# Performance work log

Measured on AMD Instinct MI355X. Metric: run time of the kernel, lower is better.

Reference implementation:

```python
import jax, jax.numpy as jnp
import numpy as np

VOCAB, HIDDEN, NUM_LABELS = 400000, 300, 7
B, S = 256, 512


def setup_inputs() -> dict:
    key = jax.random.key(0)
    ks = jax.random.split(key, 8)
    return {
        "input_ids": jax.random.randint(ks[0], (B, S), 0, VOCAB, dtype=jnp.int64 if jax.config.jax_enable_x64 else jnp.int32).astype(jnp.int32),
        "attention_masks": jax.random.randint(ks[1], (B, S), 0, 2).astype(jnp.int32),
        "labels": jax.random.randint(ks[2], (B,), 0, NUM_LABELS).astype(jnp.int32),
        "drop_mask": jax.random.randint(ks[3], (B, S), 0, 2).astype(jnp.int32),
        "emb_table": jax.random.normal(ks[4], (VOCAB, HIDDEN), dtype=jnp.float32) * 0.1,
        "W1": jax.random.normal(ks[5], (HIDDEN, HIDDEN), dtype=jnp.float32) * 0.05,
        "b1": jnp.zeros((HIDDEN,), jnp.float32),
        "W2": jax.random.normal(ks[6], (HIDDEN, HIDDEN), dtype=jnp.float32) * 0.05,
        "b2": jnp.zeros((HIDDEN,), jnp.float32),
        "W3": jax.random.normal(ks[7], (NUM_LABELS, HIDDEN), dtype=jnp.float32) * 0.05,
        "b3": jnp.zeros((NUM_LABELS,), jnp.float32),
    }


def reference(input_ids, attention_masks, labels, drop_mask, emb_table, W1, b1, W2, b2, W3, b3):
    # masked token ids (padding -> id 0), then embedding gather: [B,S,H]
    masked = input_ids * attention_masks
    embs = emb_table[masked]
    # NOTE: original's per-element torch.mul loop discards results, so the
    # dropout mask only affects the divisor via count_nonzero per row.
    nonzeros = jnp.sum(drop_mask, axis=1).astype(jnp.float32)  # [B]
    avg = jnp.sum(embs, axis=1) / nonzeros[:, None]            # [B,H]
    h = jax.nn.relu(avg @ W1.T + b1)
    h = jax.nn.relu(h @ W2.T + b2)
    logits = h @ W3.T + b3                                     # [B,7]
    logp = jax.nn.log_softmax(logits, axis=-1)
    loss = -jnp.mean(jnp.take_along_axis(logp, labels[:, None], axis=1))
    return loss, logits
```

## Files before the change

### kernel.cpp

```cpp
#include <hip/hip_runtime.h>
#include <hip/hip_bf16.h>

#define B_ 256
#define S_ 512
#define H_ 300
#define NL_ 7
#define NT_ 320
#define NCHUNK_ 4
#define SPER_ (S_ / NCHUNK_)

#define NGATHER_ (B_ * NCHUNK_)
#define NTILE_ 10
#define NTRANS_ (2 * NTILE_ * NTILE_)

__global__ __launch_bounds__(NT_) void dan_gather_t(
    const int* __restrict__ ids, const int* __restrict__ am,
    const float* __restrict__ emb,
    const float* __restrict__ W1, const float* __restrict__ W2,
    float* __restrict__ partial, float* __restrict__ WT1,
    float* __restrict__ WT2) {
  const int bid = blockIdx.x;
  const int t = threadIdx.x;

  if (bid < NGATHER_) {
    const int b = bid >> 2, c = bid & 3;
    __shared__ int cid[SPER_ + 8];
    __shared__ int wcnt[2];
    __shared__ int snnzp;

    int id = 0;
    if (t < SPER_) {
      int off = b * S_ + c * SPER_ + t;
      id = ids[off] * am[off];
    }
    for (int s = t; s < SPER_ + 8; s += NT_) cid[s] = 0;
    unsigned long long m = __ballot(id != 0);
    const int lane = t & 63;
    if (t < SPER_ && lane == 0) wcnt[t >> 6] = __popcll(m);
    __syncthreads();
    if (t < SPER_ && id != 0) {
      int base = (t >> 6) ? wcnt[0] : 0;
      int rank = __popcll(m & ((1ull << lane) - 1));
      cid[base + rank] = id;
    }
    if (t == 0) snnzp = (wcnt[0] + wcnt[1] + 7) & ~7;
    __syncthreads();

    if (t < H_) {
      const float* ep = emb + t;
      const int nnzp = snnzp;
      float a0 = 0.f, a1 = 0.f, a2 = 0.f, a3 = 0.f;
#pragma unroll 2
      for (int s = 0; s < nnzp; s += 8) {
        a0 += ep[(size_t)cid[s] * H_];
        a1 += ep[(size_t)cid[s + 1] * H_];
        a2 += ep[(size_t)cid[s + 2] * H_];
        a3 += ep[(size_t)cid[s + 3] * H_];
        a0 += ep[(size_t)cid[s + 4] * H_];
        a1 += ep[(size_t)cid[s + 5] * H_];
        a2 += ep[(size_t)cid[s + 6] * H_];
        a3 += ep[(size_t)cid[s + 7] * H_];
      }
      float r = (a0 + a1) + (a2 + a3) + (float)(SPER_ - nnzp) * ep[0];
      partial[bid * H_ + t] = r;
    }
  } else {
    int tid = bid - NGATHER_;
    const float* src = (tid < NTILE_ * NTILE_) ? W1 : W2;
    float* dst = (tid < NTILE_ * NTILE_) ? WT1 : WT2;
    int tile = (tid < NTILE_ * NTILE_) ? tid : tid - NTILE_ * NTILE_;
    int by = (tile / NTILE_) * 32, bx = (tile % NTILE_) * 32;
    __shared__ float stile[32][33];
    int tx = t & 31, ty = t >> 5;
    for (int r = ty; r < 32; r += 10) {
      int row = by + r, col = bx + tx;
      if (row < H_ && col < H_) stile[r][tx] = src[row * H_ + col];
    }
    __syncthreads();
    for (int r = ty; r < 32; r += 10) {
      int row = bx + r, col = by + tx;
      if (row < H_ && col < H_) dst[row * H_ + col] = stile[tx][r];
    }
  }
}

__global__ __launch_bounds__(NT_) void dan_mlp(
    const float* __restrict__ partial, const int* __restrict__ drop,
    const int* __restrict__ labels,
    const float* __restrict__ WT1, const float* __restrict__ b1,
    const float* __restrict__ WT2, const float* __restrict__ b2,
    const float* __restrict__ W3, const float* __restrict__ b3,
    float* __restrict__ out, float* __restrict__ perloss) {
  const int b = blockIdx.x, t = threadIdx.x;
  __shared__ float savg[H_];
  __shared__ float sh[H_];
  __shared__ float swred[NT_ / 64];
  __shared__ float snz;
  __shared__ float slog[NL_];

  int nzp = 0;
  for (int s = t; s < S_; s += NT_) nzp += drop[b * S_ + s];
  for (int o = 32; o > 0; o >>= 1) nzp += __shfl_down(nzp, o, 64);
  if ((t & 63) == 0) swred[t >> 6] = (float)nzp;
  __syncthreads();
  if (t == 0) {
    float s = 0.f;
    for (int w = 0; w < NT_ / 64; ++w) s += swred[w];
    snz = s;
  }
  __syncthreads();

  if (t < H_) {
    float s = 0.f;
#pragma unroll
    for (int c = 0; c < NCHUNK_; ++c) s += partial[(b * NCHUNK_ + c) * H_ + t];
    savg[t] = s / snz;
  }
  __syncthreads();

  if (t < H_) {
    float acc = b1[t];
    const float* w = WT1 + t;
#pragma unroll 10
    for (int j = 0; j < H_; ++j) acc = fmaf(w[(size_t)j * H_], savg[j], acc);
    sh[t] = fmaxf(acc, 0.f);
  }
  __syncthreads();

  if (t < H_) {
    float acc = b2[t];
    const float* w = WT2 + t;
#pragma unroll 10
    for (int j = 0; j < H_; ++j) acc = fmaf(w[(size_t)j * H_], sh[j], acc);
    savg[t] = fmaxf(acc, 0.f);
  }
  __syncthreads();

  if (t < NL_) {
    float acc = b3[t];
    const float* w = W3 + t * H_;
    for (int j = 0; j < H_; ++j) acc = fmaf(w[j], savg[j], acc);
    slog[t] = acc;
    out[1 + b * NL_ + t] = acc;
  }
  __syncthreads();

  if (t == 0) {
    float m = slog[0];
    for (int c = 1; c < NL_; ++c) m = fmaxf(m, slog[c]);
    float se = 0.f;
    for (int c = 0; c < NL_; ++c) se += expf(slog[c] - m);
    int lab = labels[b];
    perloss[b] = slog[lab] - m - logf(se);
  }
}

__global__ void dan_loss(const float* __restrict__ perloss,
                         float* __restrict__ out) {
  const int t = threadIdx.x;
  float v = perloss[t];
  for (int o = 32; o > 0; o >>= 1) v += __shfl_down(v, o, 64);
  __shared__ float r[4];
  if ((t & 63) == 0) r[t >> 6] = v;
  __syncthreads();
  if (t == 0) out[0] = -(r[0] + r[1] + r[2] + r[3]) * (1.0f / B_);
}

extern "C" void kernel_launch(void* const* d_in, const int* in_sizes, int n_in,
                              void* d_out, int out_size, void* d_ws,
                              size_t ws_size, hipStream_t stream) {
  const int* ids = (const int*)d_in[0];
  const int* am = (const int*)d_in[1];
  const int* labels = (const int*)d_in[2];
  const int* drop = (const int*)d_in[3];
  const float* emb = (const float*)d_in[4];
  const float* W1 = (const float*)d_in[5];
  const float* b1 = (const float*)d_in[6];
  const float* W2 = (const float*)d_in[7];
  const float* b2 = (const float*)d_in[8];
  const float* W3 = (const float*)d_in[9];
  const float* b3 = (const float*)d_in[10];
  float* out = (float*)d_out;

  float* partial = (float*)d_ws;
  float* perloss = partial + (size_t)NGATHER_ * H_;
  float* WT1 = perloss + B_;
  float* WT2 = WT1 + (size_t)H_ * H_;

  dan_gather_t<<<NGATHER_ + NTRANS_, NT_, 0, stream>>>(ids, am, emb, W1, W2,
                                                       partial, WT1, WT2);
  dan_mlp<<<B_, NT_, 0, stream>>>(partial, drop, labels, WT1, b1, WT2, b2, W3,
                                  b3, out, perloss);
  dan_loss<<<1, B_, 0, stream>>>(perloss, out);
}
```

Before: 50.77 us.

## Split gather into more chunks, drop compaction, fold loss into MLP via atomic counter

The gather stage now splits each sequence into 8 chunks instead of 4, which doubles the block count. It removes the ballot-based compaction of nonzero ids, so every token, padding included, is gathered directly with a fully unrolled loop. The transpose blocks are moved to the front of the grid, and the separate loss kernel is replaced by a last-block-done atomic counter inside the MLP kernel, which removes one launch at the cost of an extra memset. Dropping compaction means padding rows (id 0) are loaded from memory instead of being skipped. These loads are probably cached, but they add load instructions in exchange for more parallelism and less per-block setup.

```diff
diff --git a/kernel.cpp b/kernel.cpp
--- a/kernel.cpp
+++ b/kernel.cpp
@@ -6,7 +6,7 @@
 #define H_ 300
 #define NL_ 7
 #define NT_ 320
-#define NCHUNK_ 4
+#define NCHUNK_ 8
 #define SPER_ (S_ / NCHUNK_)
 
 #define NGATHER_ (B_ * NCHUNK_)
@@ -22,50 +22,33 @@
   const int bid = blockIdx.x;
   const int t = threadIdx.x;
 
-  if (bid < NGATHER_) {
-    const int b = bid >> 2, c = bid & 3;
-    __shared__ int cid[SPER_ + 8];
-    __shared__ int wcnt[2];
-    __shared__ int snnzp;
-
-    int id = 0;
+  if (bid >= NTRANS_) {
+    const int gb = bid - NTRANS_;
+    const int b = gb >> 3, c = gb & 7;
+    __shared__ int sid[SPER_];
     if (t < SPER_) {
       int off = b * S_ + c * SPER_ + t;
-      id = ids[off] * am[off];
+      sid[t] = ids[off] * am[off];
     }
-    for (int s = t; s < SPER_ + 8; s += NT_) cid[s] = 0;
-    unsigned long long m = __ballot(id != 0);
-    const int lane = t & 63;
-    if (t < SPER_ && lane == 0) wcnt[t >> 6] = __popcll(m);
     __syncthreads();
-    if (t < SPER_ && id != 0) {
-      int base = (t >> 6) ? wcnt[0] : 0;
-      int rank = __popcll(m & ((1ull << lane) - 1));
-      cid[base + rank] = id;
-    }
-    if (t == 0) snnzp = (wcnt[0] + wcnt[1] + 7) & ~7;
-    __syncthreads();
-
     if (t < H_) {
       const float* ep = emb + t;
-      const int nnzp = snnzp;
       float a0 = 0.f, a1 = 0.f, a2 = 0.f, a3 = 0.f;
-#pragma unroll 2
-      for (int s = 0; s < nnzp; s += 8) {
-        a0 += ep[(size_t)cid[s] * H_];
-        a1 += ep[(size_t)cid[s + 1] * H_];
-        a2 += ep[(size_t)cid[s + 2] * H_];
-        a3 += ep[(size_t)cid[s + 3] * H_];
-        a0 += ep[(size_t)cid[s + 4] * H_];
-        a1 += ep[(size_t)cid[s + 5] * H_];
-        a2 += ep[(size_t)cid[s + 6] * H_];
-        a3 += ep[(size_t)cid[s + 7] * H_];
+#pragma unroll
+      for (int s = 0; s < SPER_; s += 8) {
+        a0 += ep[sid[s] * H_];
+        a1 += ep[sid[s + 1] * H_];
+        a2 += ep[sid[s + 2] * H_];
+        a3 += ep[sid[s + 3] * H_];
+        a0 += ep[sid[s + 4] * H_];
+        a1 += ep[sid[s + 5] * H_];
+        a2 += ep[sid[s + 6] * H_];
+        a3 += ep[sid[s + 7] * H_];
       }
-      float r = (a0 + a1) + (a2 + a3) + (float)(SPER_ - nnzp) * ep[0];
-      partial[bid * H_ + t] = r;
+      partial[gb * H_ + t] = (a0 + a1) + (a2 + a3);
     }
   } else {
-    int tid = bid - NGATHER_;
+    int tid = bid;
     const float* src = (tid < NTILE_ * NTILE_) ? W1 : W2;
     float* dst = (tid < NTILE_ * NTILE_) ? WT1 : WT2;
     int tile = (tid < NTILE_ * NTILE_) ? tid : tid - NTILE_ * NTILE_;
@@ -90,7 +73,8 @@
     const float* __restrict__ WT1, const float* __restrict__ b1,
     const float* __restrict__ WT2, const float* __restrict__ b2,
     const float* __restrict__ W3, const float* __restrict__ b3,
-    float* __restrict__ out, float* __restrict__ perloss) {
+    float* __restrict__ out, float* __restrict__ perloss,
+    unsigned* __restrict__ cnt) {
   const int b = blockIdx.x, t = threadIdx.x;
   __shared__ float savg[H_];
   __shared__ float sh[H_];
@@ -153,17 +137,23 @@
     int lab = labels[b];
     perloss[b] = slog[lab] - m - logf(se);
   }
-}
+  __syncthreads();
 
-__global__ void dan_loss(const float* __restrict__ perloss,
-                         float* __restrict__ out) {
-  const int t = threadIdx.x;
-  float v = perloss[t];
-  for (int o = 32; o > 0; o >>= 1) v += __shfl_down(v, o, 64);
-  __shared__ float r[4];
-  if ((t & 63) == 0) r[t >> 6] = v;
-  __syncthreads();
-  if (t == 0) out[0] = -(r[0] + r[1] + r[2] + r[3]) * (1.0f / B_);
+  if (t < 64) {
+    unsigned old = 0;
+    if (t == 0) {
+      __threadfence();
+      old = atomicAdd(cnt, 1u);
+    }
+    old = __shfl(old, 0, 64);
+    if (old == B_ - 1) {
+      __threadfence();
+      float v = perloss[t] + perloss[t + 64] + perloss[t + 128] +
+                perloss[t + 192];
+      for (int o = 32; o > 0; o >>= 1) v += __shfl_xor(v, o, 64);
+      if (t == 0) out[0] = -v * (1.0f / (float)B_);
+    }
+  }
 }
 
 extern "C" void kernel_launch(void* const* d_in, const int* in_sizes, int n_in,
@@ -186,10 +176,11 @@
   float* perloss = partial + (size_t)NGATHER_ * H_;
   float* WT1 = perloss + B_;
   float* WT2 = WT1 + (size_t)H_ * H_;
+  unsigned* cnt = (unsigned*)(WT2 + (size_t)H_ * H_);
 
-  dan_gather_t<<<NGATHER_ + NTRANS_, NT_, 0, stream>>>(ids, am, emb, W1, W2,
+  hipMemsetAsync(cnt, 0, sizeof(unsigned), stream);
+  dan_gather_t<<<NTRANS_ + NGATHER_, NT_, 0, stream>>>(ids, am, emb, W1, W2,
                                                        partial, WT1, WT2);
   dan_mlp<<<B_, NT_, 0, stream>>>(partial, drop, labels, WT1, b1, WT2, b2, W3,
-                                  b3, out, perloss);
-  dan_loss<<<1, B_, 0, stream>>>(perloss, out);
+                                  b3, out, perloss, cnt);
 }
```

Measured after the change: 58.75 us. 1.16x slower.
